# Optimization experiments

Hardware: AMD Instinct MI355X
Metric: run time of the kernel (lower is better)

## Reference

```python
import jax, jax.numpy as jnp
import numpy as np

G_NUM, K_DEG = 3, 3  # grid intervals, spline order (module defaults)
LN_EPS = 1e-5


def _bspline_basis(x, grid, k):
    """Cox-de Boor B-spline basis. x: [N, D], grid: [D, G+2k+1] -> [N, D, G+k]."""
    xg = x[:, :, None]                      # [N, D, 1]
    g = grid[None, :, :]                    # [1, D, M]
    B = ((xg >= g[..., :-1]) & (xg < g[..., 1:])).astype(x.dtype)  # degree 0
    for d in range(1, k + 1):
        left = (xg - g[..., :-(d + 1)]) / (g[..., d:-1] - g[..., :-(d + 1)])
        right = (g[..., d + 1:] - xg) / (g[..., d + 1:] - g[..., 1:-d])
        B = left * B[..., :-1] + right * B[..., 1:]
    return B                                # [N, D, G+k]


def _kan_layer(x, grid, coef, scale_base, scale_sp, node_scale, node_bias):
    # spline branch: fold per-edge scale_sp into coef, contract basis without
    # materializing the [N, in, out] per-edge tensor
    basis = _bspline_basis(x, grid, K_DEG)              # [N, in, G+k]
    coef_eff = coef * scale_sp[..., None]               # [in, out, G+k]
    y = jnp.einsum('nib,iob->no', basis, coef_eff)      # spline sum over edges
    y = y + jax.nn.silu(x) @ scale_base                 # residual base function
    return node_scale * y + node_bias                   # per-node affine


def setup_inputs() -> dict:
    key = jax.random.key(0)
    ks = jax.random.split(key, 12)
    B, S = 16, 1024
    D0, D1, D2 = 256, 512, 256
    nb = G_NUM + K_DEG  # num basis fns = 6
    h = 2.0 / G_NUM
    knots = np.arange(-K_DEG, G_NUM + K_DEG + 1) * h - 1.0  # [G+2k+1]=10, range [-3,3]
    grid1 = jnp.asarray(np.tile(knots, (D0, 1)), jnp.float32)
    grid2 = jnp.asarray(np.tile(knots, (D1, 1)), jnp.float32)
    inp = {
        'x': jax.random.normal(ks[0], (B, S, D0), jnp.float32),
        'grid1': grid1,
        'coef1': jax.random.normal(ks[1], (D0, D1, nb), jnp.float32) * 0.1,
        'scale_base1': jax.random.normal(ks[2], (D0, D1), jnp.float32) / np.sqrt(D0),
        'scale_sp1': jnp.ones((D0, D1), jnp.float32),
        'node_scale1': jnp.ones((D1,), jnp.float32),
        'node_bias1': jnp.zeros((D1,), jnp.float32),
        'grid2': grid2,
        'coef2': jax.random.normal(ks[3], (D1, D2, nb), jnp.float32) * 0.1,
        'scale_base2': jax.random.normal(ks[4], (D1, D2), jnp.float32) / np.sqrt(D1),
        'scale_sp2': jnp.ones((D1, D2), jnp.float32),
        'node_scale2': jnp.ones((D2,), jnp.float32),
        'node_bias2': jnp.zeros((D2,), jnp.float32),
        'ln_gamma': jnp.ones((D2,), jnp.float32),
        'ln_beta': jnp.zeros((D2,), jnp.float32),
    }
    return inp


def reference(x, grid1, coef1, scale_base1, scale_sp1, node_scale1, node_bias1,
              grid2, coef2, scale_base2, scale_sp2, node_scale2, node_bias2,
              ln_gamma, ln_beta):
    b, s, d = x.shape
    residual = x  # start_dim == final_dim -> residual path active
    h = x.reshape(-1, d)
    h = _kan_layer(h, grid1, coef1, scale_base1, scale_sp1, node_scale1, node_bias1)
    h = _kan_layer(h, grid2, coef2, scale_base2, scale_sp2, node_scale2, node_bias2)
    h = h.reshape(b, s, -1)
    h = h + residual
    # LayerNorm over last dim
    mu = jnp.mean(h, axis=-1, keepdims=True)
    var = jnp.mean((h - mu) ** 2, axis=-1, keepdims=True)
    h = (h - mu) * jax.lax.rsqrt(var + LN_EPS) * ln_gamma + ln_beta
    # torch nn.GELU default is exact (erf) variant
    return jax.nn.gelu(h, approximate=False)
```

## Files before the change

### kernel.cpp

```cpp
#include <hip/hip_runtime.h>
#include <cstdint>
#include <cstddef>

using f16   = _Float16;
using half8 = __attribute__((ext_vector_type(8))) _Float16;
using f32x4 = __attribute__((ext_vector_type(4))) float;
using ull   = unsigned long long;

#define DINL __device__ __forceinline__

DINL void gload_lds16(const void* gptr, void* lptr) {
  __builtin_amdgcn_global_load_lds(
      reinterpret_cast<const __attribute__((address_space(1))) uint32_t*>(
          reinterpret_cast<uintptr_t>(gptr)),
      reinterpret_cast<__attribute__((address_space(3))) uint32_t*>(
          reinterpret_cast<uintptr_t>(lptr)),
      16, 0, 0);
}

DINL unsigned pkh(float a, float b) {
  unsigned short ha = __builtin_bit_cast(unsigned short, (f16)a);
  unsigned short hb = __builtin_bit_cast(unsigned short, (f16)b);
  return (unsigned)ha | ((unsigned)hb << 16);
}

struct U4 { unsigned x, y, z, w; };

DINL U4 expand_pack(float x) {
  float xs = (x + 3.0f) * 1.5f;
  float mf = floorf(xs);
  int   m  = (int)mf;
  float u = xs - mf, u2 = u * u, u3 = u2 * u, um = 1.0f - u;
  float p3 = u3 * (1.0f / 6.0f);
  float p2 = (1.0f + 3.0f * (u + u2 - u3)) * (1.0f / 6.0f);
  float p1 = (4.0f - 6.0f * u2 + 3.0f * u3) * (1.0f / 6.0f);
  float p0 = um * um * um * (1.0f / 6.0f);
  ull P = (ull)pkh(p0, p1) | ((ull)pkh(p2, p3) << 32);
  if ((unsigned)m > 8u) P = 0;
  int s    = m * 16 - 48;
  int sneg = min(63, max(0, -s));
  int spos = min(63, max(0, s));
  int shi2 = min(63, max(0, s - 64));
  ull rlo = (s < 0) ? (P >> sneg) : ((s < 64) ? (P << spos) : 0ull);
  ull rhi = (s < 0) ? 0ull
                    : ((s < 64) ? ((P >> (63 - spos)) >> 1) : (P << shi2));
  float sil = x / (1.0f + __expf(-x));
  U4 r;
  r.x = (unsigned)rlo;
  r.y = (unsigned)(rlo >> 32);
  r.z = (unsigned)rhi;
  r.w = pkh(sil, 0.0f);
  return r;
}

__global__ __launch_bounds__(256)
void prep_w_kernel(const float* __restrict__ coef, const float* __restrict__ ssp,
                   const float* __restrict__ sb, f16* __restrict__ Wt,
                   int Din, int Dout) {
  int idx = blockIdx.x * 256 + threadIdx.x;
  if (idx >= Din * Dout) return;
  int n = idx / Din;
  int d = idx - n * Din;
  float s = ssp[(size_t)d * Dout + n];
  const float* c = coef + ((size_t)d * Dout + n) * 6;
  half8 wv;
#pragma unroll
  for (int b = 0; b < 6; ++b) wv[b] = (f16)(c[b] * s);
  wv[6] = (f16)sb[(size_t)d * Dout + n];
  wv[7] = (f16)0.0f;
  int dp = (d & ~7) | ((d & 7) ^ (n & 7));
  *reinterpret_cast<half8*>(Wt + ((size_t)n * Din + dp) * 8) = wv;
}

template <bool BIAS>
__global__ __launch_bounds__(512, 4)
void kan_gemm(const float* __restrict__ X, int ldx,
              const f16* __restrict__ Wt, int ldw,
              const float* __restrict__ nscale, const float* __restrict__ nbias,
              int N, float* __restrict__ Out, int nsteps) {
  __shared__ alignas(16) f16 A0[64 * 64];
  __shared__ alignas(16) f16 A1[64 * 64];
  __shared__ alignas(16) f16 B0[256 * 64];
  __shared__ alignas(16) f16 B1[256 * 64];

  const int tid  = threadIdx.x;
  const int w    = tid >> 6;
  const int lane = tid & 63;
  const int l15  = lane & 15, l7 = lane & 7, hi = lane >> 4;
  const int wm   = w >> 2, wn = w & 3;
  const int m0   = blockIdx.y * 64;
  const int n0   = blockIdx.x * 256;
  const int dim0 = blockIdx.z * (nsteps * 8);
  float* outz = Out + (size_t)blockIdx.z * ((size_t)gridDim.y * 64) * N;

  const int ar = tid >> 3, ad = tid & 7;
  const float* asrc = X + (size_t)(m0 + ar) * ldx + dim0 + ad;
  const int aoff = ar * 64 + 8 * (ad ^ (ar & 7));

  const f16* wb[4];
  int ldsb[4];
#pragma unroll
  for (int q = 0; q < 4; ++q) {
    int c   = tid + q * 512;
    wb[q]   = Wt + (size_t)(n0 + (c >> 3)) * ldw + (size_t)dim0 * 8 + (c & 7) * 8;
    ldsb[q] = c * 8;
  }

  f32x4 acc[2][4] = {};

  auto stageB = [&](f16* buf, int k0) {
#pragma unroll
    for (int q = 0; q < 4; ++q) gload_lds16(wb[q] + k0, buf + ldsb[q]);
  };

  auto compute = [&](const f16* bA, const f16* bB) {
#pragma unroll
    for (int kk = 0; kk < 2; ++kk) {
      const int sl = kk * 4 + hi;
      half8 av[2], bv[4];
#pragma unroll
      for (int i = 0; i < 2; ++i)
        av[i] = *reinterpret_cast<const half8*>(
            bA + (wm * 32 + i * 16 + l15) * 64 + 8 * (sl ^ l7));
#pragma unroll
      for (int j = 0; j < 4; ++j)
        bv[j] = *reinterpret_cast<const half8*>(
            bB + (wn * 64 + j * 16 + l15) * 64 + 8 * (sl ^ l7));
#pragma unroll
      for (int i = 0; i < 2; ++i)
#pragma unroll
        for (int j = 0; j < 4; ++j)
          acc[i][j] = __builtin_amdgcn_mfma_f32_16x16x32_f16(av[i], bv[j], acc[i][j], 0, 0, 0);
    }
  };

  auto writeA = [&](f16* buf, U4 e) {
    *reinterpret_cast<U4*>(buf + aoff) = e;
  };

  {
    float xa = asrc[0];
    stageB(B0, 0);
    writeA(A0, expand_pack(xa));
  }
  float xn = asrc[8];
  __syncthreads();

  const float* ap = asrc + 16;
  const int npairs = (nsteps - 2) >> 1;
  int k = 64;
  for (int p = 0; p < npairs; ++p) {
    stageB(B1, k);
    float xa2 = ap[0];
    compute(A0, B0);
    writeA(A1, expand_pack(xn));
    __syncthreads();
    stageB(B0, k + 64);
    xn = ap[8];
    compute(A1, B1);
    writeA(A0, expand_pack(xa2));
    __syncthreads();
    ap += 16;
    k  += 128;
  }

  stageB(B1, k);
  compute(A0, B0);
  writeA(A1, expand_pack(xn));
  __syncthreads();
  compute(A1, B1);

#pragma unroll
  for (int j = 0; j < 4; ++j) {
    int col   = n0 + wn * 64 + j * 16 + l15;
    float nsv = nscale[col];
    float nbv = BIAS ? nbias[col] : 0.0f;
#pragma unroll
    for (int i = 0; i < 2; ++i) {
      int rb = m0 + wm * 32 + i * 16 + hi * 4;
#pragma unroll
      for (int r = 0; r < 4; ++r)
        outz[(size_t)(rb + r) * N + col] = nsv * acc[i][j][r] + nbv;
    }
  }
}

__global__ __launch_bounds__(256)
void ln_gelu_kernel(const float* __restrict__ P0, const float* __restrict__ P1,
                    const float* __restrict__ X,  const float* __restrict__ nb2,
                    const float* __restrict__ gamma, const float* __restrict__ beta,
                    float* __restrict__ out, int rows) {
  int row  = blockIdx.x * 4 + (threadIdx.x >> 6);
  int lane = threadIdx.x & 63;
  if (row >= rows) return;
  const float4 a  = *reinterpret_cast<const float4*>(P0 + (size_t)row * 256 + lane * 4);
  const float4 b  = *reinterpret_cast<const float4*>(P1 + (size_t)row * 256 + lane * 4);
  const float4 xr = *reinterpret_cast<const float4*>(X  + (size_t)row * 256 + lane * 4);
  const float4 nb = *reinterpret_cast<const float4*>(nb2 + lane * 4);
  const float4 g  = *reinterpret_cast<const float4*>(gamma + lane * 4);
  const float4 be = *reinterpret_cast<const float4*>(beta + lane * 4);
  float h[4] = { a.x + b.x + nb.x + xr.x, a.y + b.y + nb.y + xr.y,
                 a.z + b.z + nb.z + xr.z, a.w + b.w + nb.w + xr.w };
  float s = h[0] + h[1] + h[2] + h[3];
#pragma unroll
  for (int o = 32; o >= 1; o >>= 1) s += __shfl_xor(s, o);
  float mu = s * (1.0f / 256.0f);
  float vs = 0.f;
#pragma unroll
  for (int j = 0; j < 4; ++j) { float d = h[j] - mu; vs += d * d; }
#pragma unroll
  for (int o = 32; o >= 1; o >>= 1) vs += __shfl_xor(vs, o);
  float inv = rsqrtf(vs * (1.0f / 256.0f) + 1e-5f);
  float o4[4];
#pragma unroll
  for (int j = 0; j < 4; ++j) {
    float gj = (&g.x)[j], bj = (&be.x)[j];
    float v = (h[j] - mu) * inv * gj + bj;
    o4[j] = 0.5f * v * (1.0f + erff(v * 0.70710678118654752f));
  }
  *reinterpret_cast<float4*>(out + (size_t)row * 256 + lane * 4) =
      make_float4(o4[0], o4[1], o4[2], o4[3]);
}

extern "C" void kernel_launch(void* const* d_in, const int* in_sizes, int n_in,
                              void* d_out, int out_size, void* d_ws, size_t ws_size,
                              hipStream_t stream) {
  (void)in_sizes; (void)n_in; (void)out_size; (void)ws_size;
  const float* x     = (const float*)d_in[0];
  const float* coef1 = (const float*)d_in[2];
  const float* sb1   = (const float*)d_in[3];
  const float* ssp1  = (const float*)d_in[4];
  const float* ns1   = (const float*)d_in[5];
  const float* nb1   = (const float*)d_in[6];
  const float* coef2 = (const float*)d_in[8];
  const float* sb2   = (const float*)d_in[9];
  const float* ssp2  = (const float*)d_in[10];
  const float* ns2   = (const float*)d_in[11];
  const float* nb2   = (const float*)d_in[12];
  const float* lgam  = (const float*)d_in[13];
  const float* lbet  = (const float*)d_in[14];
  float* out = (float*)d_out;

  const int Ntok = 16 * 1024;
  const int D0 = 256, D1 = 512, D2 = 256;

  char*  ws   = (char*)d_ws;
  float* h1   = (float*)ws;
  size_t off  = (size_t)Ntok * D1 * sizeof(float);
  float* part = (float*)(ws + off);
  off += (size_t)2 * Ntok * D2 * sizeof(float);
  f16* Wt1 = (f16*)(ws + off);
  off += (size_t)D1 * D0 * 8 * sizeof(f16);
  f16* Wt2 = (f16*)(ws + off);

  prep_w_kernel<<<(D0 * D1 + 255) / 256, 256, 0, stream>>>(coef1, ssp1, sb1, Wt1, D0, D1);
  prep_w_kernel<<<(D1 * D2 + 255) / 256, 256, 0, stream>>>(coef2, ssp2, sb2, Wt2, D1, D2);

  kan_gemm<true><<<dim3(D1 / 256, Ntok / 64, 1), 512, 0, stream>>>(
      x, D0, Wt1, D0 * 8, ns1, nb1, D1, h1, D0 / 8);

  kan_gemm<false><<<dim3(D2 / 256, Ntok / 64, 2), 512, 0, stream>>>(
      h1, D1, Wt2, D1 * 8, ns2, nullptr, D2, part, D1 / 16);

  ln_gelu_kernel<<<Ntok / 4, 256, 0, stream>>>(
      part, part + (size_t)Ntok * D2, x, nb2, lgam, lbet, out, Ntok);
}
```

Before: 123.8 us.

## Store intermediate activations and split-K partials in fp16, raise MFMA wave priority

The hidden layer h1 and the two split-K partial outputs now go to workspace in fp16 instead of fp32, which halves the global memory traffic between the two GEMMs and the LayerNorm/GELU kernel. The GEMM is templated on input and output types so it converts on load and store. The compute section also raises wave priority with s_setprio around the MFMA block. The cost is extra rounding of intermediates to fp16, and larger h1 values could lose precision or overflow.

```diff
diff --git a/kernel.cpp b/kernel.cpp
--- a/kernel.cpp
+++ b/kernel.cpp
@@ -3,6 +3,7 @@
 #include <cstddef>
 
 using f16   = _Float16;
+using half4 = __attribute__((ext_vector_type(4))) _Float16;
 using half8 = __attribute__((ext_vector_type(8))) _Float16;
 using f32x4 = __attribute__((ext_vector_type(4))) float;
 using ull   = unsigned long long;
@@ -72,12 +73,12 @@
   *reinterpret_cast<half8*>(Wt + ((size_t)n * Din + dp) * 8) = wv;
 }
 
-template <bool BIAS>
+template <bool BIAS, typename TIN, typename TOUT>
 __global__ __launch_bounds__(512, 4)
-void kan_gemm(const float* __restrict__ X, int ldx,
+void kan_gemm(const TIN* __restrict__ X, int ldx,
               const f16* __restrict__ Wt, int ldw,
               const float* __restrict__ nscale, const float* __restrict__ nbias,
-              int N, float* __restrict__ Out, int nsteps) {
+              int N, TOUT* __restrict__ Out, int nsteps) {
   __shared__ alignas(16) f16 A0[64 * 64];
   __shared__ alignas(16) f16 A1[64 * 64];
   __shared__ alignas(16) f16 B0[256 * 64];
@@ -91,10 +92,10 @@
   const int m0   = blockIdx.y * 64;
   const int n0   = blockIdx.x * 256;
   const int dim0 = blockIdx.z * (nsteps * 8);
-  float* outz = Out + (size_t)blockIdx.z * ((size_t)gridDim.y * 64) * N;
+  TOUT* outz = Out + (size_t)blockIdx.z * ((size_t)gridDim.y * 64) * N;
 
   const int ar = tid >> 3, ad = tid & 7;
-  const float* asrc = X + (size_t)(m0 + ar) * ldx + dim0 + ad;
+  const TIN* asrc = X + (size_t)(m0 + ar) * ldx + dim0 + ad;
   const int aoff = ar * 64 + 8 * (ad ^ (ar & 7));
 
   const f16* wb[4];
@@ -114,6 +115,7 @@
   };
 
   auto compute = [&](const f16* bA, const f16* bB) {
+    __builtin_amdgcn_s_setprio(1);
 #pragma unroll
     for (int kk = 0; kk < 2; ++kk) {
       const int sl = kk * 4 + hi;
@@ -132,6 +134,7 @@
         for (int j = 0; j < 4; ++j)
           acc[i][j] = __builtin_amdgcn_mfma_f32_16x16x32_f16(av[i], bv[j], acc[i][j], 0, 0, 0);
     }
+    __builtin_amdgcn_s_setprio(0);
   };
 
   auto writeA = [&](f16* buf, U4 e) {
@@ -139,24 +142,24 @@
   };
 
   {
-    float xa = asrc[0];
+    float xa = (float)asrc[0];
     stageB(B0, 0);
     writeA(A0, expand_pack(xa));
   }
-  float xn = asrc[8];
+  float xn = (float)asrc[8];
   __syncthreads();
 
-  const float* ap = asrc + 16;
+  const TIN* ap = asrc + 16;
   const int npairs = (nsteps - 2) >> 1;
   int k = 64;
   for (int p = 0; p < npairs; ++p) {
     stageB(B1, k);
-    float xa2 = ap[0];
+    float xa2 = (float)ap[0];
     compute(A0, B0);
     writeA(A1, expand_pack(xn));
     __syncthreads();
     stageB(B0, k + 64);
-    xn = ap[8];
+    xn = (float)ap[8];
     compute(A1, B1);
     writeA(A0, expand_pack(xa2));
     __syncthreads();
@@ -180,27 +183,29 @@
       int rb = m0 + wm * 32 + i * 16 + hi * 4;
 #pragma unroll
       for (int r = 0; r < 4; ++r)
-        outz[(size_t)(rb + r) * N + col] = nsv * acc[i][j][r] + nbv;
+        outz[(size_t)(rb + r) * N + col] = (TOUT)(nsv * acc[i][j][r] + nbv);
     }
   }
 }
 
 __global__ __launch_bounds__(256)
-void ln_gelu_kernel(const float* __restrict__ P0, const float* __restrict__ P1,
+void ln_gelu_kernel(const f16* __restrict__ P0, const f16* __restrict__ P1,
                     const float* __restrict__ X,  const float* __restrict__ nb2,
                     const float* __restrict__ gamma, const float* __restrict__ beta,
                     float* __restrict__ out, int rows) {
   int row  = blockIdx.x * 4 + (threadIdx.x >> 6);
   int lane = threadIdx.x & 63;
   if (row >= rows) return;
-  const float4 a  = *reinterpret_cast<const float4*>(P0 + (size_t)row * 256 + lane * 4);
-  const float4 b  = *reinterpret_cast<const float4*>(P1 + (size_t)row * 256 + lane * 4);
+  const half4  a4 = *reinterpret_cast<const half4*>(P0 + (size_t)row * 256 + lane * 4);
+  const half4  b4 = *reinterpret_cast<const half4*>(P1 + (size_t)row * 256 + lane * 4);
   const float4 xr = *reinterpret_cast<const float4*>(X  + (size_t)row * 256 + lane * 4);
   const float4 nb = *reinterpret_cast<const float4*>(nb2 + lane * 4);
   const float4 g  = *reinterpret_cast<const float4*>(gamma + lane * 4);
   const float4 be = *reinterpret_cast<const float4*>(beta + lane * 4);
-  float h[4] = { a.x + b.x + nb.x + xr.x, a.y + b.y + nb.y + xr.y,
-                 a.z + b.z + nb.z + xr.z, a.w + b.w + nb.w + xr.w };
+  float h[4];
+#pragma unroll
+  for (int j = 0; j < 4; ++j)
+    h[j] = (float)a4[j] + (float)b4[j] + (&nb.x)[j] + (&xr.x)[j];
   float s = h[0] + h[1] + h[2] + h[3];
 #pragma unroll
   for (int o = 32; o >= 1; o >>= 1) s += __shfl_xor(s, o);
@@ -214,8 +219,7 @@
   float o4[4];
 #pragma unroll
   for (int j = 0; j < 4; ++j) {
-    float gj = (&g.x)[j], bj = (&be.x)[j];
-    float v = (h[j] - mu) * inv * gj + bj;
+    float v = (h[j] - mu) * inv * (&g.x)[j] + (&be.x)[j];
     o4[j] = 0.5f * v * (1.0f + erff(v * 0.70710678118654752f));
   }
   *reinterpret_cast<float4*>(out + (size_t)row * 256 + lane * 4) =
@@ -244,11 +248,11 @@
   const int Ntok = 16 * 1024;
   const int D0 = 256, D1 = 512, D2 = 256;
 
-  char*  ws   = (char*)d_ws;
-  float* h1   = (float*)ws;
-  size_t off  = (size_t)Ntok * D1 * sizeof(float);
-  float* part = (float*)(ws + off);
-  off += (size_t)2 * Ntok * D2 * sizeof(float);
+  char* ws    = (char*)d_ws;
+  f16*  h1    = (f16*)ws;
+  size_t off  = (size_t)Ntok * D1 * sizeof(f16);
+  f16*  part  = (f16*)(ws + off);
+  off += (size_t)2 * Ntok * D2 * sizeof(f16);
   f16* Wt1 = (f16*)(ws + off);
   off += (size_t)D1 * D0 * 8 * sizeof(f16);
   f16* Wt2 = (f16*)(ws + off);
@@ -256,10 +260,10 @@
   prep_w_kernel<<<(D0 * D1 + 255) / 256, 256, 0, stream>>>(coef1, ssp1, sb1, Wt1, D0, D1);
   prep_w_kernel<<<(D1 * D2 + 255) / 256, 256, 0, stream>>>(coef2, ssp2, sb2, Wt2, D1, D2);
 
-  kan_gemm<true><<<dim3(D1 / 256, Ntok / 64, 1), 512, 0, stream>>>(
+  kan_gemm<true, float, f16><<<dim3(D1 / 256, Ntok / 64, 1), 512, 0, stream>>>(
       x, D0, Wt1, D0 * 8, ns1, nb1, D1, h1, D0 / 8);
 
-  kan_gemm<false><<<dim3(D2 / 256, Ntok / 64, 2), 512, 0, stream>>>(
+  kan_gemm<false, f16, f16><<<dim3(D2 / 256, Ntok / 64, 2), 512, 0, stream>>>(
       h1, D1, Wt2, D1 * 8, ns2, nullptr, D2, part, D1 / 16);
 
   ln_gelu_kernel<<<Ntok / 4, 256, 0, stream>>>(
```

After: 118.6 us. 1.04x faster.
